# Kernel tuning notes

Hardware: AMD Instinct MI355X
Metric: run time of the kernel (lower is better)

Reference implementation:

```python
import jax, jax.numpy as jnp
import numpy as np

HID = 256
SLOTS = 64
K = 2
TAU = 8.0
EPS = 1e-5


def setup_inputs() -> dict:
    key = jax.random.key(0)
    ks = jax.random.split(key, 8)
    B, T = 512, 256
    s = lambda fan_in: 1.0 / np.sqrt(fan_in)
    return {
        "x": jax.random.uniform(ks[0], (B, T, 1), jnp.float32, 0.0, 10.0),
        "W_embed": jax.random.uniform(ks[1], (HID, 1), jnp.float32, -1.0, 1.0),
        "b_embed": jax.random.uniform(ks[2], (HID,), jnp.float32, -1.0, 1.0),
        "W_update": jax.random.uniform(ks[3], (HID, HID), jnp.float32, -s(HID), s(HID)),
        "b_update": jax.random.uniform(ks[4], (HID,), jnp.float32, -s(HID), s(HID)),
        "gamma": jnp.ones((HID,), jnp.float32),
        "beta": jnp.zeros((HID,), jnp.float32),
        "W_out": jax.random.uniform(ks[5], (10, HID), jnp.float32, -s(HID), s(HID)),
        "b_out": jax.random.uniform(ks[6], (10,), jnp.float32, -s(HID), s(HID)),
        "context_strength": jnp.float32(0.2),
    }


def _gaussian_attention(pointer, num_positions):
    # pointer: [B] float. Returns indices [B,5] int32, weights [B,5] float.
    offsets = jnp.arange(-K, K + 1)
    base = jnp.clip(jnp.floor(pointer).astype(jnp.int32), 0, num_positions - 1)
    indices = (base[:, None] + offsets[None, :]) % num_positions
    delta = indices.astype(pointer.dtype) - pointer[:, None]
    weights = jax.nn.softmax(-(delta ** 2) / TAU, axis=1)
    return indices, weights


def reference(x, W_embed, b_embed, W_update, b_update, gamma, beta, W_out, b_out, context_strength):
    B, T, _ = x.shape
    cs = jax.nn.sigmoid(context_strength)

    def step(carry, x_t):
        h, memory, pointer = carry  # [B,H], [B,SLOTS,H], [B]
        inp = jnp.tanh(x_t @ W_embed.T + b_embed)           # [B,H]
        indices, weights = _gaussian_attention(pointer, SLOTS)
        neighborhood = jnp.take_along_axis(memory, indices[:, :, None], axis=1)  # [B,5,H]
        context = jnp.einsum('bk,bkh->bh', weights, neighborhood)
        combined = inp + cs * context
        h = jnp.tanh((combined + h) @ W_update.T + b_update)
        mu = jnp.mean(h, axis=-1, keepdims=True)
        var = jnp.mean((h - mu) ** 2, axis=-1, keepdims=True)
        h = (h - mu) * jax.lax.rsqrt(var + EPS) * gamma + beta
        contribution = weights[:, :, None] * h[:, None, :]   # [B,5,H]
        memory = jax.vmap(lambda m, i, c: m.at[i].add(c))(memory, indices, contribution)
        pointer = (pointer + 1.0) % SLOTS
        return (h, memory, pointer), None

    h0 = jnp.zeros((B, HID), x.dtype)
    mem0 = jnp.zeros((B, SLOTS, HID), x.dtype)
    ptr0 = jnp.zeros((B,), x.dtype)
    (h, _, _), _ = jax.lax.scan(step, (h0, mem0, ptr0), jnp.swapaxes(x, 0, 1))
    return h @ W_out.T + b_out
```

## Files before the change

kernel.cpp:

```cpp
#include <hip/hip_runtime.h>


#define TT 256

typedef __bf16 bf16x8 __attribute__((ext_vector_type(8)));
typedef float  f32x4  __attribute__((ext_vector_type(4)));

__device__ __forceinline__ float fast_tanh(float x) {
    float e = __expf(2.f * x);
    return 1.f - __fdividef(2.f, e + 1.f);
}

template<int CTRL, int RM>
__device__ __forceinline__ float dpp_add(float v) {
    int t = __builtin_amdgcn_update_dpp(0, __float_as_int(v), CTRL, RM, 0xf, true);
    return v + __int_as_float(t);
}
__device__ __forceinline__ float wave_sum63(float v) {
    v = dpp_add<0xB1,  0xf>(v);
    v = dpp_add<0x4E,  0xf>(v);
    v = dpp_add<0x141, 0xf>(v);
    v = dpp_add<0x140, 0xf>(v);
    v = dpp_add<0x142, 0xa>(v);
    v = dpp_add<0x143, 0xc>(v);
    return v;
}

#define SMEM_BYTES 138416

__global__ __launch_bounds__(512, 2)
void postnorm_kernel(const float* __restrict__ x,
                     const float* __restrict__ W_embed,
                     const float* __restrict__ b_embed,
                     const float* __restrict__ W_update,
                     const float* __restrict__ b_update,
                     const float* __restrict__ gamma,
                     const float* __restrict__ beta,
                     const float* __restrict__ W_out,
                     const float* __restrict__ b_out,
                     const float* __restrict__ ctx_s,
                     float* __restrict__ out)
{
    extern __shared__ __align__(16) char smem[];
    float*  s_mem  = (float*)(smem);
    float*  s_x    = (float*)(smem + 131072);
    float*  s_y    = (float*)(smem + 133120);
    __bf16* s_v    = (__bf16*)(smem + 135168);
    float*  s_red1 = (float*)(smem + 136224);
    float*  s_red2 = (float*)(smem + 136256);
    float*  s_wt   = (float*)(smem + 136288);
    float*  s_oacc = (float*)(smem + 138336);

    const int tid  = threadIdx.x;
    const int n    = tid >> 8;
    const int i    = tid & 255;
    const int wave = tid >> 6;
    const int lane = tid & 63;
    const int bn   = lane & 15;
    const int quad = lane >> 4;
    const int r0   = blockIdx.x * 2;

    {   f32x4 z = {0.f, 0.f, 0.f, 0.f};
        f32x4* p = (f32x4*)s_mem;
        #pragma unroll
        for (int k = 0; k < 16; ++k) p[tid + k * 512] = z;
    }
    if (tid < 264) ((unsigned int*)s_v)[tid] = 0u;
    s_x[tid] = x[(r0 + n) * TT + i];
    if (tid < 20) s_oacc[tid] = 0.f;

    if (tid < 64) {
        float wv[5]; float ssum = 0.f;
        #pragma unroll
        for (int k = 0; k < 5; ++k) {
            int idx = (tid + k - 2) & 63;
            float d = (float)idx - (float)tid;
            wv[k] = expf(-(d * d) * 0.125f);
            ssum += wv[k];
        }
        #pragma unroll
        for (int k = 0; k < 5; ++k) s_wt[tid * 8 + k] = wv[k] / ssum;
    }

    const float we  = W_embed[i];
    const float be  = b_embed[i];
    const float bu  = b_update[i];
    const float gm  = gamma[i];
    const float btt = beta[i];
    const float csv = 1.f / (1.f + expf(-ctx_s[0]));

    bf16x8 wfa[2][8];
    #pragma unroll
    for (int mt = 0; mt < 2; ++mt) {
        #pragma unroll
        for (int kt = 0; kt < 8; ++kt) {
            const float* wp = W_update + (wave * 32 + mt * 16 + bn) * 256
                                       + kt * 32 + quad * 8;
            f32x4 a = *(const f32x4*)wp;
            f32x4 b = *(const f32x4*)(wp + 4);
            bf16x8 f;
            f[0] = (__bf16)a[0]; f[1] = (__bf16)a[1];
            f[2] = (__bf16)a[2]; f[3] = (__bf16)a[3];
            f[4] = (__bf16)b[0]; f[5] = (__bf16)b[1];
            f[6] = (__bf16)b[2]; f[7] = (__bf16)b[3];
            wfa[mt][kt] = f;
        }
    }

    __syncthreads();
    {
        float inp = fast_tanh(s_x[n * 256] * we + be);
        s_v[n * 264 + i] = (__bf16)inp;
    }

    float wt0, wt1, wt2, wt3, wt4;
    {   f32x4 wv = *(const f32x4*)(s_wt);
        wt0 = wv[0]; wt1 = wv[1]; wt2 = wv[2]; wt3 = wv[3]; wt4 = s_wt[4];
    }
    __syncthreads();

    float hn = 0.f;
    float w0 = 0.f, w1 = 0.f, w2 = 0.f, w3 = 0.f, w4 = 0.f;
    float* mcol = s_mem + (n << 14) + i;
    const __bf16* vsrc = s_v + (bn & 1) * 264 + quad * 8;

    #pragma unroll 1
    for (int t = 0; t < TT; ++t) {
        f32x4 a0a = {0,0,0,0}, a0b = {0,0,0,0}, a1a = {0,0,0,0}, a1b = {0,0,0,0};
        #pragma unroll
        for (int kt = 0; kt < 4; ++kt) {
            bf16x8 bfr0 = *(const bf16x8*)(vsrc + kt * 32);
            bf16x8 bfr1 = *(const bf16x8*)(vsrc + (kt + 4) * 32);
            a0a = __builtin_amdgcn_mfma_f32_16x16x32_bf16(wfa[0][kt],     bfr0, a0a, 0, 0, 0);
            a1a = __builtin_amdgcn_mfma_f32_16x16x32_bf16(wfa[1][kt],     bfr0, a1a, 0, 0, 0);
            a0b = __builtin_amdgcn_mfma_f32_16x16x32_bf16(wfa[0][kt + 4], bfr1, a0b, 0, 0, 0);
            a1b = __builtin_amdgcn_mfma_f32_16x16x32_bf16(wfa[1][kt + 4], bfr1, a1b, 0, 0, 0);
        }
        if (bn < 2) {
            f32x4 y0 = a0a + a0b, y1 = a1a + a1b;
            float* yb = s_y + bn * 256 + wave * 32 + quad * 4;
            *(f32x4*)yb        = y0;
            *(f32x4*)(yb + 16) = y1;
        }
        __syncthreads();

        float yt = fast_tanh(s_y[tid] + bu);
        float s1 = wave_sum63(yt);
        float s2 = wave_sum63(yt * yt);
        if (lane == 63) { s_red1[wave] = s1; s_red2[wave] = s2; }
        __syncthreads();

        f32x4 r1 = *(const f32x4*)(s_red1 + n * 4);
        f32x4 r2 = *(const f32x4*)(s_red2 + n * 4);
        float S1 = (r1[0] + r1[1]) + (r1[2] + r1[3]);
        float S2 = (r2[0] + r2[1]) + (r2[2] + r2[3]);
        float mu   = S1 * (1.f / 256.f);
        float var  = S2 * (1.f / 256.f) - mu * mu;
        float rstd = rsqrtf(var + 1e-5f);
        hn = (yt - mu) * rstd * gm + btt;

        w0 += wt0 * hn; w1 += wt1 * hn; w2 += wt2 * hn;
        w3 += wt3 * hn; w4 += wt4 * hn;

        if (t < TT - 1) {
            mcol[((t - 2) & 63) << 8] = w0;
            float nf = mcol[((t + 3) & 63) << 8];
            w0 = w1; w1 = w2; w2 = w3; w3 = w4; w4 = nf;
            f32x4 nw = *(const f32x4*)(s_wt + ((t + 1) & 63) * 8);
            float nw4 = s_wt[((t + 1) & 63) * 8 + 4];
            float ctx = ((nw[0] * w0 + nw[1] * w1) + (nw[2] * w2 + nw[3] * w3))
                      + nw4 * w4;
            float inp = fast_tanh(s_x[n * 256 + t + 1] * we + be);
            float v = inp + csv * ctx + hn;
            s_v[n * 264 + i] = (__bf16)v;
            wt0 = nw[0]; wt1 = nw[1]; wt2 = nw[2]; wt3 = nw[3]; wt4 = nw4;
        }
        __syncthreads();
    }

    #pragma unroll
    for (int o = 0; o < 10; ++o) {
        float p = hn * W_out[o * 256 + i];
        #pragma unroll
        for (int m = 32; m >= 1; m >>= 1) p += __shfl_xor(p, m, 64);
        if (lane == 0) atomicAdd(&s_oacc[n * 10 + o], p);
    }
    __syncthreads();
    if (tid < 20) {
        int nn = tid / 10, o = tid % 10;
        out[(r0 + nn) * 10 + o] = s_oacc[tid] + b_out[o];
    }
}

extern "C" void kernel_launch(void* const* d_in, const int* in_sizes, int n_in,
                              void* d_out, int out_size, void* d_ws, size_t ws_size,
                              hipStream_t stream) {
    const float* x    = (const float*)d_in[0];
    const float* W_e  = (const float*)d_in[1];
    const float* b_e  = (const float*)d_in[2];
    const float* W_u  = (const float*)d_in[3];
    const float* b_u  = (const float*)d_in[4];
    const float* gmm  = (const float*)d_in[5];
    const float* bta  = (const float*)d_in[6];
    const float* W_o  = (const float*)d_in[7];
    const float* b_o  = (const float*)d_in[8];
    const float* cst  = (const float*)d_in[9];
    float* out = (float*)d_out;

    (void)hipFuncSetAttribute(reinterpret_cast<const void*>(postnorm_kernel),
                              hipFuncAttributeMaxDynamicSharedMemorySize,
                              SMEM_BYTES);

    postnorm_kernel<<<dim3(256), dim3(512), SMEM_BYTES, stream>>>(
        x, W_e, b_e, W_u, b_u, gmm, bta, W_o, b_o, cst, out);
}
```

Baseline: 319.7 us.

## Process one batch row per block and apply tanh directly on MFMA outputs

Each block now handles one batch row with 256 threads instead of two rows with 512, so each wave holds 64 output rows of bf16 weights in registers and issues 32 MFMAs per step. The tanh and the partial LayerNorm sums are computed directly from the MFMA accumulators, which removes the s_y round-trip and one __syncthreads per timestep. Memory and weight loads for the next step are hoisted ahead of the MFMA chain to hide LDS latency. In exchange each wave holds twice as many weight registers, and the batch size of one wastes MFMA columns; the grid doubles to 512 blocks with half the shared memory each.

```diff
diff --git a/kernel.cpp b/kernel.cpp
--- a/kernel.cpp
+++ b/kernel.cpp
@@ -26,9 +26,9 @@
     return v;
 }
 
-#define SMEM_BYTES 138416
-
-__global__ __launch_bounds__(512, 2)
+#define SMEM_BYTES 70240
+
+__global__ __launch_bounds__(256, 2)
 void postnorm_kernel(const float* __restrict__ x,
                      const float* __restrict__ W_embed,
                      const float* __restrict__ b_embed,
@@ -43,31 +43,29 @@
 {
     extern __shared__ __align__(16) char smem[];
     float*  s_mem  = (float*)(smem);
-    float*  s_x    = (float*)(smem + 131072);
-    float*  s_y    = (float*)(smem + 133120);
-    __bf16* s_v    = (__bf16*)(smem + 135168);
-    float*  s_red1 = (float*)(smem + 136224);
-    float*  s_red2 = (float*)(smem + 136256);
-    float*  s_wt   = (float*)(smem + 136288);
-    float*  s_oacc = (float*)(smem + 138336);
+    float*  s_x    = (float*)(smem + 65536);
+    float*  s_yt   = (float*)(smem + 66560);
+    __bf16* s_v    = (__bf16*)(smem + 67584);
+    float*  s_red1 = (float*)(smem + 68096);
+    float*  s_red2 = (float*)(smem + 68112);
+    float*  s_wt   = (float*)(smem + 68128);
+    float*  s_oacc = (float*)(smem + 70176);
 
     const int tid  = threadIdx.x;
-    const int n    = tid >> 8;
-    const int i    = tid & 255;
+    const int i    = tid;
     const int wave = tid >> 6;
     const int lane = tid & 63;
     const int bn   = lane & 15;
     const int quad = lane >> 4;
-    const int r0   = blockIdx.x * 2;
+    const int r    = blockIdx.x;
 
     {   f32x4 z = {0.f, 0.f, 0.f, 0.f};
         f32x4* p = (f32x4*)s_mem;
         #pragma unroll
-        for (int k = 0; k < 16; ++k) p[tid + k * 512] = z;
-    }
-    if (tid < 264) ((unsigned int*)s_v)[tid] = 0u;
-    s_x[tid] = x[(r0 + n) * TT + i];
-    if (tid < 20) s_oacc[tid] = 0.f;
+        for (int k = 0; k < 16; ++k) p[tid + k * 256] = z;
+    }
+    s_x[tid] = x[r * TT + tid];
+    if (tid < 10) s_oacc[tid] = 0.f;
 
     if (tid < 64) {
         float wv[5]; float ssum = 0.f;
@@ -84,17 +82,18 @@
 
     const float we  = W_embed[i];
     const float be  = b_embed[i];
-    const float bu  = b_update[i];
     const float gm  = gamma[i];
     const float btt = beta[i];
     const float csv = 1.f / (1.f + expf(-ctx_s[0]));
 
-    bf16x8 wfa[2][8];
+    const f32x4 bu4 = *(const f32x4*)(b_update + wave * 64 + (bn & 3) * 16 + quad * 4);
+
+    bf16x8 wfa[4][8];
     #pragma unroll
-    for (int mt = 0; mt < 2; ++mt) {
+    for (int mt = 0; mt < 4; ++mt) {
         #pragma unroll
         for (int kt = 0; kt < 8; ++kt) {
-            const float* wp = W_update + (wave * 32 + mt * 16 + bn) * 256
+            const float* wp = W_update + (wave * 64 + mt * 16 + bn) * 256
                                        + kt * 32 + quad * 8;
             f32x4 a = *(const f32x4*)wp;
             f32x4 b = *(const f32x4*)(wp + 4);
@@ -109,10 +108,9 @@
 
     __syncthreads();
     {
-        float inp = fast_tanh(s_x[n * 256] * we + be);
-        s_v[n * 264 + i] = (__bf16)inp;
-    }
-
+        float inp = fast_tanh(s_x[0] * we + be);
+        s_v[i] = (__bf16)inp;
+    }
     float wt0, wt1, wt2, wt3, wt4;
     {   f32x4 wv = *(const f32x4*)(s_wt);
         wt0 = wv[0]; wt1 = wv[1]; wt2 = wv[2]; wt3 = wv[3]; wt4 = s_wt[4];
@@ -121,37 +119,48 @@
 
     float hn = 0.f;
     float w0 = 0.f, w1 = 0.f, w2 = 0.f, w3 = 0.f, w4 = 0.f;
-    float* mcol = s_mem + (n << 14) + i;
-    const __bf16* vsrc = s_v + (bn & 1) * 264 + quad * 8;
+    float* mcol = s_mem + i;
+    const __bf16* vsrc = s_v + quad * 8;
 
     #pragma unroll 1
     for (int t = 0; t < TT; ++t) {
-        f32x4 a0a = {0,0,0,0}, a0b = {0,0,0,0}, a1a = {0,0,0,0}, a1b = {0,0,0,0};
-        #pragma unroll
-        for (int kt = 0; kt < 4; ++kt) {
-            bf16x8 bfr0 = *(const bf16x8*)(vsrc + kt * 32);
-            bf16x8 bfr1 = *(const bf16x8*)(vsrc + (kt + 4) * 32);
-            a0a = __builtin_amdgcn_mfma_f32_16x16x32_bf16(wfa[0][kt],     bfr0, a0a, 0, 0, 0);
-            a1a = __builtin_amdgcn_mfma_f32_16x16x32_bf16(wfa[1][kt],     bfr0, a1a, 0, 0, 0);
-            a0b = __builtin_amdgcn_mfma_f32_16x16x32_bf16(wfa[0][kt + 4], bfr1, a0b, 0, 0, 0);
-            a1b = __builtin_amdgcn_mfma_f32_16x16x32_bf16(wfa[1][kt + 4], bfr1, a1b, 0, 0, 0);
-        }
-        if (bn < 2) {
-            f32x4 y0 = a0a + a0b, y1 = a1a + a1b;
-            float* yb = s_y + bn * 256 + wave * 32 + quad * 4;
-            *(f32x4*)yb        = y0;
-            *(f32x4*)(yb + 16) = y1;
+        const int tn = (t < TT - 1) ? t + 1 : 0;
+        float nf  = mcol[((t + 3) & 63) << 8];
+        f32x4 nw  = *(const f32x4*)(s_wt + (tn & 63) * 8);
+        float nw4 = s_wt[(tn & 63) * 8 + 4];
+        float xN  = s_x[tn];
+
+        f32x4 a0 = {0,0,0,0}, a1 = {0,0,0,0}, a2 = {0,0,0,0}, a3 = {0,0,0,0};
+        #pragma unroll
+        for (int kt = 0; kt < 8; ++kt) {
+            bf16x8 bfr = *(const bf16x8*)(vsrc + kt * 32);
+            a0 = __builtin_amdgcn_mfma_f32_16x16x32_bf16(wfa[0][kt], bfr, a0, 0, 0, 0);
+            a1 = __builtin_amdgcn_mfma_f32_16x16x32_bf16(wfa[1][kt], bfr, a1, 0, 0, 0);
+            a2 = __builtin_amdgcn_mfma_f32_16x16x32_bf16(wfa[2][kt], bfr, a2, 0, 0, 0);
+            a3 = __builtin_amdgcn_mfma_f32_16x16x32_bf16(wfa[3][kt], bfr, a3, 0, 0, 0);
+        }
+        f32x4 sel = (bn == 0) ? a0 : (bn == 1) ? a1 : (bn == 2) ? a2 : a3;
+        float y0 = fast_tanh(sel[0] + bu4[0]);
+        float y1 = fast_tanh(sel[1] + bu4[1]);
+        float y2 = fast_tanh(sel[2] + bu4[2]);
+        float y3 = fast_tanh(sel[3] + bu4[3]);
+        float s1 = (y0 + y1) + (y2 + y3);
+        float s2 = ((y0 * y0 + y1 * y1) + (y2 * y2 + y3 * y3));
+        const bool act = (bn < 4);
+        s1 = act ? s1 : 0.f;
+        s2 = act ? s2 : 0.f;
+        s1 = wave_sum63(s1);
+        s2 = wave_sum63(s2);
+        if (lane == 63) { s_red1[wave] = s1; s_red2[wave] = s2; }
+        if (act) {
+            f32x4 ytv = {y0, y1, y2, y3};
+            *(f32x4*)(s_yt + wave * 64 + bn * 16 + quad * 4) = ytv;
         }
         __syncthreads();
 
-        float yt = fast_tanh(s_y[tid] + bu);
-        float s1 = wave_sum63(yt);
-        float s2 = wave_sum63(yt * yt);
-        if (lane == 63) { s_red1[wave] = s1; s_red2[wave] = s2; }
-        __syncthreads();
-
-        f32x4 r1 = *(const f32x4*)(s_red1 + n * 4);
-        f32x4 r2 = *(const f32x4*)(s_red2 + n * 4);
+        f32x4 r1 = *(const f32x4*)s_red1;
+        f32x4 r2 = *(const f32x4*)s_red2;
+        float yt = s_yt[i];
         float S1 = (r1[0] + r1[1]) + (r1[2] + r1[3]);
         float S2 = (r2[0] + r2[1]) + (r2[2] + r2[3]);
         float mu   = S1 * (1.f / 256.f);
@@ -164,15 +173,12 @@
 
         if (t < TT - 1) {
             mcol[((t - 2) & 63) << 8] = w0;
-            float nf = mcol[((t + 3) & 63) << 8];
             w0 = w1; w1 = w2; w2 = w3; w3 = w4; w4 = nf;
-            f32x4 nw = *(const f32x4*)(s_wt + ((t + 1) & 63) * 8);
-            float nw4 = s_wt[((t + 1) & 63) * 8 + 4];
             float ctx = ((nw[0] * w0 + nw[1] * w1) + (nw[2] * w2 + nw[3] * w3))
                       + nw4 * w4;
-            float inp = fast_tanh(s_x[n * 256 + t + 1] * we + be);
+            float inp = fast_tanh(xN * we + be);
             float v = inp + csv * ctx + hn;
-            s_v[n * 264 + i] = (__bf16)v;
+            s_v[i] = (__bf16)v;
             wt0 = nw[0]; wt1 = nw[1]; wt2 = nw[2]; wt3 = nw[3]; wt4 = nw4;
         }
         __syncthreads();
@@ -180,16 +186,11 @@
 
     #pragma unroll
     for (int o = 0; o < 10; ++o) {
-        float p = hn * W_out[o * 256 + i];
-        #pragma unroll
-        for (int m = 32; m >= 1; m >>= 1) p += __shfl_xor(p, m, 64);
-        if (lane == 0) atomicAdd(&s_oacc[n * 10 + o], p);
+        float p = wave_sum63(hn * W_out[o * 256 + i]);
+        if (lane == 63) atomicAdd(&s_oacc[o], p);
     }
     __syncthreads();
-    if (tid < 20) {
-        int nn = tid / 10, o = tid % 10;
-        out[(r0 + nn) * 10 + o] = s_oacc[tid] + b_out[o];
-    }
+    if (tid < 10) out[r * 10 + tid] = s_oacc[tid] + b_out[tid];
 }
 
 extern "C" void kernel_launch(void* const* d_in, const int* in_sizes, int n_in,
@@ -211,6 +212,6 @@
                               hipFuncAttributeMaxDynamicSharedMemorySize,
                               SMEM_BYTES);
 
-    postnorm_kernel<<<dim3(256), dim3(512), SMEM_BYTES, stream>>>(
+    postnorm_kernel<<<dim3(512), dim3(256), SMEM_BYTES, stream>>>(
         x, W_e, b_e, W_u, b_u, gmm, bta, W_o, b_o, cst, out);
 }
```

New measurement: 378.3 us. 18.3% more time.

## Halve block size to four waves, each owning 64 output rows for both batch rows

Applied to the files above, without the earlier changes.

The block drops from 512 to 256 threads. Each wave now holds 64 rows of W_update in registers (4x8 bf16 fragments) and computes the matvec for both batch rows. Each thread handles both rows' hidden unit. Tanh and the layernorm partial sums are now computed directly from the MFMA accumulators, so one barrier round-trip for the y values is no longer needed. The attention weights are computed in registers instead of read from a shared table. In exchange, register pressure doubles, the block has fewer waves to hide latency, and each thread does twice the per-element work.

```diff
diff --git a/kernel.cpp b/kernel.cpp
--- a/kernel.cpp
+++ b/kernel.cpp
@@ -26,9 +26,23 @@
     return v;
 }
 
-#define SMEM_BYTES 138416
-
-__global__ __launch_bounds__(512, 2)
+__device__ __forceinline__ void attn_w(int p, float w[5]) {
+    float s = 0.f;
+    #pragma unroll
+    for (int k = 0; k < 5; ++k) {
+        int idx = (p + k - 2) & 63;
+        float d = (float)(idx - p);
+        w[k] = expf(-(d * d) * 0.125f);
+        s += w[k];
+    }
+    float inv = 1.f / s;
+    #pragma unroll
+    for (int k = 0; k < 5; ++k) w[k] *= inv;
+}
+
+#define SMEM_BYTES 136576
+
+__global__ __launch_bounds__(256, 1)
 void postnorm_kernel(const float* __restrict__ x,
                      const float* __restrict__ W_embed,
                      const float* __restrict__ b_embed,
@@ -43,18 +57,16 @@
 {
     extern __shared__ __align__(16) char smem[];
     float*  s_mem  = (float*)(smem);
-    float*  s_x    = (float*)(smem + 131072);
-    float*  s_y    = (float*)(smem + 133120);
+    float*  s_yt   = (float*)(smem + 131072);
+    float*  s_x    = (float*)(smem + 133120);
     __bf16* s_v    = (__bf16*)(smem + 135168);
-    float*  s_red1 = (float*)(smem + 136224);
-    float*  s_red2 = (float*)(smem + 136256);
-    float*  s_wt   = (float*)(smem + 136288);
-    float*  s_oacc = (float*)(smem + 138336);
+    float*  s_red1 = (float*)(smem + 136192);
+    float*  s_red2 = (float*)(smem + 136224);
+    float*  s_part = (float*)(smem + 136256);
 
     const int tid  = threadIdx.x;
-    const int n    = tid >> 8;
-    const int i    = tid & 255;
-    const int wave = tid >> 6;
+    const int i    = tid;
+    const int w    = tid >> 6;
     const int lane = tid & 63;
     const int bn   = lane & 15;
     const int quad = lane >> 4;
@@ -63,38 +75,32 @@
     {   f32x4 z = {0.f, 0.f, 0.f, 0.f};
         f32x4* p = (f32x4*)s_mem;
         #pragma unroll
-        for (int k = 0; k < 16; ++k) p[tid + k * 512] = z;
-    }
-    if (tid < 264) ((unsigned int*)s_v)[tid] = 0u;
-    s_x[tid] = x[(r0 + n) * TT + i];
-    if (tid < 20) s_oacc[tid] = 0.f;
-
-    if (tid < 64) {
-        float wv[5]; float ssum = 0.f;
-        #pragma unroll
-        for (int k = 0; k < 5; ++k) {
-            int idx = (tid + k - 2) & 63;
-            float d = (float)idx - (float)tid;
-            wv[k] = expf(-(d * d) * 0.125f);
-            ssum += wv[k];
-        }
-        #pragma unroll
-        for (int k = 0; k < 5; ++k) s_wt[tid * 8 + k] = wv[k] / ssum;
-    }
+        for (int k = 0; k < 32; ++k) p[tid + k * 256] = z;
+    }
+    s_x[i]       = x[r0 * TT + i];
+    s_x[256 + i] = x[(r0 + 1) * TT + i];
 
     const float we  = W_embed[i];
     const float be  = b_embed[i];
-    const float bu  = b_update[i];
     const float gm  = gamma[i];
     const float btt = beta[i];
-    const float csv = 1.f / (1.f + expf(-ctx_s[0]));
-
-    bf16x8 wfa[2][8];
-    #pragma unroll
-    for (int mt = 0; mt < 2; ++mt) {
+    const float cs  = 1.f / (1.f + expf(-ctx_s[0]));
+
+    float Wi[5], wt[5];
+    attn_w(30, Wi);
+    attn_w(0,  wt);
+
+    f32x4 bu4[4];
+    #pragma unroll
+    for (int mt = 0; mt < 4; ++mt)
+        bu4[mt] = *(const f32x4*)(b_update + w * 64 + mt * 16 + quad * 4);
+
+    bf16x8 wfa[4][8];
+    #pragma unroll
+    for (int mt = 0; mt < 4; ++mt) {
         #pragma unroll
         for (int kt = 0; kt < 8; ++kt) {
-            const float* wp = W_update + (wave * 32 + mt * 16 + bn) * 256
+            const float* wp = W_update + (w * 64 + mt * 16 + bn) * 256
                                        + kt * 32 + quad * 8;
             f32x4 a = *(const f32x4*)wp;
             f32x4 b = *(const f32x4*)(wp + 4);
@@ -109,86 +115,120 @@
 
     __syncthreads();
     {
-        float inp = fast_tanh(s_x[n * 256] * we + be);
-        s_v[n * 264 + i] = (__bf16)inp;
-    }
-
-    float wt0, wt1, wt2, wt3, wt4;
-    {   f32x4 wv = *(const f32x4*)(s_wt);
-        wt0 = wv[0]; wt1 = wv[1]; wt2 = wv[2]; wt3 = wv[3]; wt4 = s_wt[4];
+        float x00 = s_x[0], x01 = s_x[256];
+        s_v[i]       = (__bf16)fast_tanh(x00 * we + be);
+        s_v[256 + i] = (__bf16)fast_tanh(x01 * we + be);
     }
     __syncthreads();
 
-    float hn = 0.f;
-    float w0 = 0.f, w1 = 0.f, w2 = 0.f, w3 = 0.f, w4 = 0.f;
-    float* mcol = s_mem + (n << 14) + i;
-    const __bf16* vsrc = s_v + (bn & 1) * 264 + quad * 8;
+    float hn0 = 0.f, hn1 = 0.f;
+    float a0=0,a1=0,a2=0,a3=0,a4=0;
+    float c0=0,c1=0,c2=0,c3=0,c4=0;
+    const __bf16* vsrc = s_v + (bn & 1) * 256 + quad * 8;
 
     #pragma unroll 1
     for (int t = 0; t < TT; ++t) {
-        f32x4 a0a = {0,0,0,0}, a0b = {0,0,0,0}, a1a = {0,0,0,0}, a1b = {0,0,0,0};
-        #pragma unroll
-        for (int kt = 0; kt < 4; ++kt) {
-            bf16x8 bfr0 = *(const bf16x8*)(vsrc + kt * 32);
-            bf16x8 bfr1 = *(const bf16x8*)(vsrc + (kt + 4) * 32);
-            a0a = __builtin_amdgcn_mfma_f32_16x16x32_bf16(wfa[0][kt],     bfr0, a0a, 0, 0, 0);
-            a1a = __builtin_amdgcn_mfma_f32_16x16x32_bf16(wfa[1][kt],     bfr0, a1a, 0, 0, 0);
-            a0b = __builtin_amdgcn_mfma_f32_16x16x32_bf16(wfa[0][kt + 4], bfr1, a0b, 0, 0, 0);
-            a1b = __builtin_amdgcn_mfma_f32_16x16x32_bf16(wfa[1][kt + 4], bfr1, a1b, 0, 0, 0);
-        }
+        const int tn = (t < TT - 1) ? t + 1 : TT - 1;
+        float adm0 = s_mem[(((t + 3) & 63) << 8) + i];
+        float adm1 = s_mem[16384 + (((t + 3) & 63) << 8) + i];
+        float xn0  = s_x[tn];
+        float xn1  = s_x[256 + tn];
+        float nw0, nw1, nw2, nw3, nw4;
+        {   int pn = tn & 63;
+            if (pn >= 2 && pn <= 61) {
+                nw0 = Wi[0]; nw1 = Wi[1]; nw2 = Wi[2]; nw3 = Wi[3]; nw4 = Wi[4];
+            } else {
+                float tmp[5]; attn_w(pn, tmp);
+                nw0 = tmp[0]; nw1 = tmp[1]; nw2 = tmp[2]; nw3 = tmp[3]; nw4 = tmp[4];
+            }
+        }
+
+        f32x4 acc0 = {0,0,0,0}, acc1 = {0,0,0,0}, acc2 = {0,0,0,0}, acc3 = {0,0,0,0};
+        #pragma unroll
+        for (int kt = 0; kt < 8; ++kt) {
+            bf16x8 bfr = *(const bf16x8*)(vsrc + kt * 32);
+            acc0 = __builtin_amdgcn_mfma_f32_16x16x32_bf16(wfa[0][kt], bfr, acc0, 0, 0, 0);
+            acc1 = __builtin_amdgcn_mfma_f32_16x16x32_bf16(wfa[1][kt], bfr, acc1, 0, 0, 0);
+            acc2 = __builtin_amdgcn_mfma_f32_16x16x32_bf16(wfa[2][kt], bfr, acc2, 0, 0, 0);
+            acc3 = __builtin_amdgcn_mfma_f32_16x16x32_bf16(wfa[3][kt], bfr, acc3, 0, 0, 0);
+        }
+        f32x4 y0, y1, y2, y3;
+        float s1 = 0.f, s2 = 0.f;
+        #pragma unroll
+        for (int e = 0; e < 4; ++e) {
+            y0[e] = fast_tanh(acc0[e] + bu4[0][e]);
+            y1[e] = fast_tanh(acc1[e] + bu4[1][e]);
+            y2[e] = fast_tanh(acc2[e] + bu4[2][e]);
+            y3[e] = fast_tanh(acc3[e] + bu4[3][e]);
+            s1 += (y0[e] + y1[e]) + (y2[e] + y3[e]);
+            s2 += (y0[e]*y0[e] + y1[e]*y1[e]) + (y2[e]*y2[e] + y3[e]*y3[e]);
+        }
+        s1 += __shfl_xor(s1, 16, 64); s1 += __shfl_xor(s1, 32, 64);
+        s2 += __shfl_xor(s2, 16, 64); s2 += __shfl_xor(s2, 32, 64);
+        if (quad == 0 && bn < 2) { s_red1[bn*4 + w] = s1; s_red2[bn*4 + w] = s2; }
         if (bn < 2) {
-            f32x4 y0 = a0a + a0b, y1 = a1a + a1b;
-            float* yb = s_y + bn * 256 + wave * 32 + quad * 4;
-            *(f32x4*)yb        = y0;
+            float* yb = s_yt + bn * 256 + w * 64 + quad * 4;
+            *(f32x4*)(yb)      = y0;
             *(f32x4*)(yb + 16) = y1;
+            *(f32x4*)(yb + 32) = y2;
+            *(f32x4*)(yb + 48) = y3;
         }
         __syncthreads();
 
-        float yt = fast_tanh(s_y[tid] + bu);
-        float s1 = wave_sum63(yt);
-        float s2 = wave_sum63(yt * yt);
-        if (lane == 63) { s_red1[wave] = s1; s_red2[wave] = s2; }
+        f32x4 q1a = *(const f32x4*)(s_red1);
+        f32x4 q1b = *(const f32x4*)(s_red1 + 4);
+        f32x4 q2a = *(const f32x4*)(s_red2);
+        f32x4 q2b = *(const f32x4*)(s_red2 + 4);
+        float yt0 = s_yt[i];
+        float yt1 = s_yt[256 + i];
+        float S1a = (q1a[0]+q1a[1]) + (q1a[2]+q1a[3]);
+        float S2a = (q2a[0]+q2a[1]) + (q2a[2]+q2a[3]);
+        float S1b = (q1b[0]+q1b[1]) + (q1b[2]+q1b[3]);
+        float S2b = (q2b[0]+q2b[1]) + (q2b[2]+q2b[3]);
+        float mu0 = S1a * (1.f/256.f);
+        float mu1 = S1b * (1.f/256.f);
+        float rs0 = rsqrtf(S2a * (1.f/256.f) - mu0*mu0 + 1e-5f);
+        float rs1 = rsqrtf(S2b * (1.f/256.f) - mu1*mu1 + 1e-5f);
+        hn0 = (yt0 - mu0) * rs0 * gm + btt;
+        hn1 = (yt1 - mu1) * rs1 * gm + btt;
+
+        a0 += wt[0]*hn0; a1 += wt[1]*hn0; a2 += wt[2]*hn0; a3 += wt[3]*hn0; a4 += wt[4]*hn0;
+        c0 += wt[0]*hn1; c1 += wt[1]*hn1; c2 += wt[2]*hn1; c3 += wt[3]*hn1; c4 += wt[4]*hn1;
+
+        if (t < TT - 1) {
+            const int ret = ((t - 2) & 63) << 8;
+            s_mem[ret + i]         = a0;
+            s_mem[16384 + ret + i] = c0;
+            a0=a1; a1=a2; a2=a3; a3=a4; a4=adm0;
+            c0=c1; c1=c2; c2=c3; c3=c4; c4=adm1;
+            float ctx0 = ((nw0*a0 + nw1*a1) + (nw2*a2 + nw3*a3)) + nw4*a4;
+            float ctx1 = ((nw0*c0 + nw1*c1) + (nw2*c2 + nw3*c3)) + nw4*c4;
+            float v0 = fast_tanh(xn0 * we + be) + cs * ctx0 + hn0;
+            float v1 = fast_tanh(xn1 * we + be) + cs * ctx1 + hn1;
+            s_v[i]       = (__bf16)v0;
+            s_v[256 + i] = (__bf16)v1;
+            wt[0]=nw0; wt[1]=nw1; wt[2]=nw2; wt[3]=nw3; wt[4]=nw4;
+        }
         __syncthreads();
-
-        f32x4 r1 = *(const f32x4*)(s_red1 + n * 4);
-        f32x4 r2 = *(const f32x4*)(s_red2 + n * 4);
-        float S1 = (r1[0] + r1[1]) + (r1[2] + r1[3]);
-        float S2 = (r2[0] + r2[1]) + (r2[2] + r2[3]);
-        float mu   = S1 * (1.f / 256.f);
-        float var  = S2 * (1.f / 256.f) - mu * mu;
-        float rstd = rsqrtf(var + 1e-5f);
-        hn = (yt - mu) * rstd * gm + btt;
-
-        w0 += wt0 * hn; w1 += wt1 * hn; w2 += wt2 * hn;
-        w3 += wt3 * hn; w4 += wt4 * hn;
-
-        if (t < TT - 1) {
-            mcol[((t - 2) & 63) << 8] = w0;
-            float nf = mcol[((t + 3) & 63) << 8];
-            w0 = w1; w1 = w2; w2 = w3; w3 = w4; w4 = nf;
-            f32x4 nw = *(const f32x4*)(s_wt + ((t + 1) & 63) * 8);
-            float nw4 = s_wt[((t + 1) & 63) * 8 + 4];
-            float ctx = ((nw[0] * w0 + nw[1] * w1) + (nw[2] * w2 + nw[3] * w3))
-                      + nw4 * w4;
-            float inp = fast_tanh(s_x[n * 256 + t + 1] * we + be);
-            float v = inp + csv * ctx + hn;
-            s_v[n * 264 + i] = (__bf16)v;
-            wt0 = nw[0]; wt1 = nw[1]; wt2 = nw[2]; wt3 = nw[3]; wt4 = nw4;
-        }
-        __syncthreads();
     }
 
     #pragma unroll
     for (int o = 0; o < 10; ++o) {
-        float p = hn * W_out[o * 256 + i];
-        #pragma unroll
-        for (int m = 32; m >= 1; m >>= 1) p += __shfl_xor(p, m, 64);
-        if (lane == 0) atomicAdd(&s_oacc[n * 10 + o], p);
+        float wo = W_out[o * 256 + i];
+        float p0 = wave_sum63(hn0 * wo);
+        float p1 = wave_sum63(hn1 * wo);
+        if (lane == 63) {
+            s_part[(w*2 + 0)*10 + o] = p0;
+            s_part[(w*2 + 1)*10 + o] = p1;
+        }
     }
     __syncthreads();
     if (tid < 20) {
-        int nn = tid / 10, o = tid % 10;
-        out[(r0 + nn) * 10 + o] = s_oacc[tid] + b_out[o];
+        int n = tid / 10, o = tid % 10;
+        float r = b_out[o];
+        #pragma unroll
+        for (int ww = 0; ww < 4; ++ww) r += s_part[(ww*2 + n)*10 + o];
+        out[(r0 + n)*10 + o] = r;
     }
 }
 
@@ -211,6 +251,6 @@
                               hipFuncAttributeMaxDynamicSharedMemorySize,
                               SMEM_BYTES);
 
-    postnorm_kernel<<<dim3(256), dim3(512), SMEM_BYTES, stream>>>(
+    postnorm_kernel<<<dim3(256), dim3(256), SMEM_BYTES, stream>>>(
         x, W_e, b_e, W_u, b_u, gmm, bta, W_o, b_o, cst, out);
 }
```

After: 473.7 us. 1.48x slower.

## Fuse bias+tanh and LayerNorm partial sums into MFMA epilogue, drop one barrier

Applied to the files above, without the earlier changes.

Applies bias and tanh and computes the LayerNorm partial sums directly on the MFMA accumulator lanes, then stores the activated values. This removes one of the three per-step block barriers and the separate 63-lane wave reduction pass. It also replaces the shared-memory attention-weight table with register constants for interior pointer positions, hoists the memory and x loads ahead of the MFMA chain, and merges the split accumulators into a single chain per tile. The trade-off is a longer dependent MFMA chain and some redundant tanh work on lanes whose results are discarded.

```diff
diff --git a/kernel.cpp b/kernel.cpp
--- a/kernel.cpp
+++ b/kernel.cpp
@@ -26,7 +26,21 @@
     return v;
 }
 
-#define SMEM_BYTES 138416
+__device__ __forceinline__ void attn_w(int p, float w[5]) {
+    float s = 0.f;
+    #pragma unroll
+    for (int k = 0; k < 5; ++k) {
+        int idx = (p + k - 2) & 63;
+        float d = (float)(idx - p);
+        w[k] = expf(-(d * d) * 0.125f);
+        s += w[k];
+    }
+    float inv = 1.f / s;
+    #pragma unroll
+    for (int k = 0; k < 5; ++k) w[k] *= inv;
+}
+
+#define SMEM_BYTES 136400
 
 __global__ __launch_bounds__(512, 2)
 void postnorm_kernel(const float* __restrict__ x,
@@ -43,18 +57,17 @@
 {
     extern __shared__ __align__(16) char smem[];
     float*  s_mem  = (float*)(smem);
-    float*  s_x    = (float*)(smem + 131072);
-    float*  s_y    = (float*)(smem + 133120);
+    float*  s_yt   = (float*)(smem + 131072);
+    float*  s_x    = (float*)(smem + 133120);
     __bf16* s_v    = (__bf16*)(smem + 135168);
-    float*  s_red1 = (float*)(smem + 136224);
+    float*  s_red1 = (float*)(smem + 136192);
     float*  s_red2 = (float*)(smem + 136256);
-    float*  s_wt   = (float*)(smem + 136288);
-    float*  s_oacc = (float*)(smem + 138336);
+    float*  s_oacc = (float*)(smem + 136320);
 
     const int tid  = threadIdx.x;
     const int n    = tid >> 8;
     const int i    = tid & 255;
-    const int wave = tid >> 6;
+    const int w    = tid >> 6;
     const int lane = tid & 63;
     const int bn   = lane & 15;
     const int quad = lane >> 4;
@@ -65,36 +78,31 @@
         #pragma unroll
         for (int k = 0; k < 16; ++k) p[tid + k * 512] = z;
     }
-    if (tid < 264) ((unsigned int*)s_v)[tid] = 0u;
     s_x[tid] = x[(r0 + n) * TT + i];
     if (tid < 20) s_oacc[tid] = 0.f;
 
-    if (tid < 64) {
-        float wv[5]; float ssum = 0.f;
-        #pragma unroll
-        for (int k = 0; k < 5; ++k) {
-            int idx = (tid + k - 2) & 63;
-            float d = (float)idx - (float)tid;
-            wv[k] = expf(-(d * d) * 0.125f);
-            ssum += wv[k];
-        }
-        #pragma unroll
-        for (int k = 0; k < 5; ++k) s_wt[tid * 8 + k] = wv[k] / ssum;
-    }
-
     const float we  = W_embed[i];
     const float be  = b_embed[i];
-    const float bu  = b_update[i];
     const float gm  = gamma[i];
     const float btt = beta[i];
-    const float csv = 1.f / (1.f + expf(-ctx_s[0]));
+    const float cs  = 1.f / (1.f + expf(-ctx_s[0]));
+
+    float Wi[5];
+    attn_w(30, Wi);
+    float wt0, wt1, wt2, wt3, wt4;
+    {   float t0[5]; attn_w(0, t0);
+        wt0 = t0[0]; wt1 = t0[1]; wt2 = t0[2]; wt3 = t0[3]; wt4 = t0[4];
+    }
+
+    const f32x4 bu0 = *(const f32x4*)(b_update + w * 32 + quad * 4);
+    const f32x4 bu1 = *(const f32x4*)(b_update + w * 32 + 16 + quad * 4);
 
     bf16x8 wfa[2][8];
     #pragma unroll
     for (int mt = 0; mt < 2; ++mt) {
         #pragma unroll
         for (int kt = 0; kt < 8; ++kt) {
-            const float* wp = W_update + (wave * 32 + mt * 16 + bn) * 256
+            const float* wp = W_update + (w * 32 + mt * 16 + bn) * 256
                                        + kt * 32 + quad * 8;
             f32x4 a = *(const f32x4*)wp;
             f32x4 b = *(const f32x4*)(wp + 4);
@@ -109,81 +117,92 @@
 
     __syncthreads();
     {
-        float inp = fast_tanh(s_x[n * 256] * we + be);
-        s_v[n * 264 + i] = (__bf16)inp;
-    }
-
-    float wt0, wt1, wt2, wt3, wt4;
-    {   f32x4 wv = *(const f32x4*)(s_wt);
-        wt0 = wv[0]; wt1 = wv[1]; wt2 = wv[2]; wt3 = wv[3]; wt4 = s_wt[4];
+        float inp = fast_tanh(s_x[n << 8] * we + be);
+        s_v[tid] = (__bf16)inp;
     }
     __syncthreads();
 
     float hn = 0.f;
     float w0 = 0.f, w1 = 0.f, w2 = 0.f, w3 = 0.f, w4 = 0.f;
     float* mcol = s_mem + (n << 14) + i;
-    const __bf16* vsrc = s_v + (bn & 1) * 264 + quad * 8;
+    const __bf16* vsrc = s_v + (bn & 1) * 256 + quad * 8;
 
     #pragma unroll 1
     for (int t = 0; t < TT; ++t) {
-        f32x4 a0a = {0,0,0,0}, a0b = {0,0,0,0}, a1a = {0,0,0,0}, a1b = {0,0,0,0};
-        #pragma unroll
-        for (int kt = 0; kt < 4; ++kt) {
-            bf16x8 bfr0 = *(const bf16x8*)(vsrc + kt * 32);
-            bf16x8 bfr1 = *(const bf16x8*)(vsrc + (kt + 4) * 32);
-            a0a = __builtin_amdgcn_mfma_f32_16x16x32_bf16(wfa[0][kt],     bfr0, a0a, 0, 0, 0);
-            a1a = __builtin_amdgcn_mfma_f32_16x16x32_bf16(wfa[1][kt],     bfr0, a1a, 0, 0, 0);
-            a0b = __builtin_amdgcn_mfma_f32_16x16x32_bf16(wfa[0][kt + 4], bfr1, a0b, 0, 0, 0);
-            a1b = __builtin_amdgcn_mfma_f32_16x16x32_bf16(wfa[1][kt + 4], bfr1, a1b, 0, 0, 0);
-        }
-        if (bn < 2) {
-            f32x4 y0 = a0a + a0b, y1 = a1a + a1b;
-            float* yb = s_y + bn * 256 + wave * 32 + quad * 4;
-            *(f32x4*)yb        = y0;
+        const int tn = (t < TT - 1) ? t + 1 : TT - 1;
+        float adm = mcol[((t + 3) & 63) << 8];
+        float xn  = s_x[(n << 8) + tn];
+        float nw0, nw1, nw2, nw3, nw4;
+        {   int pn = tn & 63;
+            if (pn >= 2 && pn <= 61) {
+                nw0 = Wi[0]; nw1 = Wi[1]; nw2 = Wi[2]; nw3 = Wi[3]; nw4 = Wi[4];
+            } else {
+                float tmp[5]; attn_w(pn, tmp);
+                nw0 = tmp[0]; nw1 = tmp[1]; nw2 = tmp[2]; nw3 = tmp[3]; nw4 = tmp[4];
+            }
+        }
+
+        f32x4 acc0 = {0,0,0,0}, acc1 = {0,0,0,0};
+        #pragma unroll
+        for (int kt = 0; kt < 8; ++kt) {
+            bf16x8 bfr = *(const bf16x8*)(vsrc + kt * 32);
+            acc0 = __builtin_amdgcn_mfma_f32_16x16x32_bf16(wfa[0][kt], bfr, acc0, 0, 0, 0);
+            acc1 = __builtin_amdgcn_mfma_f32_16x16x32_bf16(wfa[1][kt], bfr, acc1, 0, 0, 0);
+        }
+        f32x4 y0, y1;
+        float s1 = 0.f, s2 = 0.f;
+        #pragma unroll
+        for (int e = 0; e < 4; ++e) {
+            y0[e] = fast_tanh(acc0[e] + bu0[e]);
+            y1[e] = fast_tanh(acc1[e] + bu1[e]);
+            s1 += y0[e] + y1[e];
+            s2 += y0[e]*y0[e] + y1[e]*y1[e];
+        }
+        const bool act = (bn < 2);
+        s1 = act ? s1 : 0.f;
+        s2 = act ? s2 : 0.f;
+        s1 += __shfl_xor(s1, 16, 64); s1 += __shfl_xor(s1, 32, 64);
+        s2 += __shfl_xor(s2, 16, 64); s2 += __shfl_xor(s2, 32, 64);
+        if (quad == 0 && act) { s_red1[bn*8 + w] = s1; s_red2[bn*8 + w] = s2; }
+        if (act) {
+            float* yb = s_yt + bn * 256 + w * 32 + quad * 4;
+            *(f32x4*)(yb)      = y0;
             *(f32x4*)(yb + 16) = y1;
         }
         __syncthreads();
 
-        float yt = fast_tanh(s_y[tid] + bu);
-        float s1 = wave_sum63(yt);
-        float s2 = wave_sum63(yt * yt);
-        if (lane == 63) { s_red1[wave] = s1; s_red2[wave] = s2; }
-        __syncthreads();
-
-        f32x4 r1 = *(const f32x4*)(s_red1 + n * 4);
-        f32x4 r2 = *(const f32x4*)(s_red2 + n * 4);
-        float S1 = (r1[0] + r1[1]) + (r1[2] + r1[3]);
-        float S2 = (r2[0] + r2[1]) + (r2[2] + r2[3]);
-        float mu   = S1 * (1.f / 256.f);
-        float var  = S2 * (1.f / 256.f) - mu * mu;
+        f32x4 q1a = *(const f32x4*)(s_red1 + n*8);
+        f32x4 q1b = *(const f32x4*)(s_red1 + n*8 + 4);
+        f32x4 q2a = *(const f32x4*)(s_red2 + n*8);
+        f32x4 q2b = *(const f32x4*)(s_red2 + n*8 + 4);
+        float yt = s_yt[tid];
+        float S1 = ((q1a[0]+q1a[1]) + (q1a[2]+q1a[3]))
+                 + ((q1b[0]+q1b[1]) + (q1b[2]+q1b[3]));
+        float S2 = ((q2a[0]+q2a[1]) + (q2a[2]+q2a[3]))
+                 + ((q2b[0]+q2b[1]) + (q2b[2]+q2b[3]));
+        float mu   = S1 * (1.f/256.f);
+        float var  = S2 * (1.f/256.f) - mu*mu;
         float rstd = rsqrtf(var + 1e-5f);
         hn = (yt - mu) * rstd * gm + btt;
 
-        w0 += wt0 * hn; w1 += wt1 * hn; w2 += wt2 * hn;
-        w3 += wt3 * hn; w4 += wt4 * hn;
+        w0 += wt0*hn; w1 += wt1*hn; w2 += wt2*hn; w3 += wt3*hn; w4 += wt4*hn;
 
         if (t < TT - 1) {
             mcol[((t - 2) & 63) << 8] = w0;
-            float nf = mcol[((t + 3) & 63) << 8];
-            w0 = w1; w1 = w2; w2 = w3; w3 = w4; w4 = nf;
-            f32x4 nw = *(const f32x4*)(s_wt + ((t + 1) & 63) * 8);
-            float nw4 = s_wt[((t + 1) & 63) * 8 + 4];
-            float ctx = ((nw[0] * w0 + nw[1] * w1) + (nw[2] * w2 + nw[3] * w3))
-                      + nw4 * w4;
-            float inp = fast_tanh(s_x[n * 256 + t + 1] * we + be);
-            float v = inp + csv * ctx + hn;
-            s_v[n * 264 + i] = (__bf16)v;
-            wt0 = nw[0]; wt1 = nw[1]; wt2 = nw[2]; wt3 = nw[3]; wt4 = nw4;
+            w0 = w1; w1 = w2; w2 = w3; w3 = w4; w4 = adm;
+            float ctx = ((nw0*w0 + nw1*w1) + (nw2*w2 + nw3*w3)) + nw4*w4;
+            float inp = fast_tanh(xn * we + be);
+            float v = inp + cs * ctx + hn;
+            s_v[tid] = (__bf16)v;
+            wt0 = nw0; wt1 = nw1; wt2 = nw2; wt3 = nw3; wt4 = nw4;
         }
         __syncthreads();
     }
 
     #pragma unroll
     for (int o = 0; o < 10; ++o) {
-        float p = hn * W_out[o * 256 + i];
-        #pragma unroll
-        for (int m = 32; m >= 1; m >>= 1) p += __shfl_xor(p, m, 64);
-        if (lane == 0) atomicAdd(&s_oacc[n * 10 + o], p);
+        float p = wave_sum63(hn * W_out[o * 256 + i]);
+        if (lane == 63) atomicAdd(&s_oacc[n * 10 + o], p);
     }
     __syncthreads();
     if (tid < 20) {
```

After: 453.6 us. 41.9% more time.
